# Kernel tuning notes

Measured on AMD Instinct MI355X. Metric: run time of the kernel, lower is better.

The kernel has to match this reference:

```python
import jax, jax.numpy as jnp
import numpy as np

N, F, K, E = 65536, 256, 8, 2097152  # nodes, feat dim, experts, edges (avg degree 32)


def setup_inputs() -> dict:
    key = jax.random.key(0)
    ks = jax.random.split(key, 7)
    x = jax.random.normal(ks[0], (N, F), dtype=jnp.float32)
    h0 = jax.random.normal(ks[1], (N, F), dtype=jnp.float32)
    z = jax.random.uniform(ks[2], (N, K), dtype=jnp.float32)
    rows = jax.random.randint(ks[3], (E,), 0, N, dtype=jnp.int32)
    cols = jax.random.randint(ks[4], (E,), 0, N, dtype=jnp.int32)
    # normalized-ish edge weights (like sym-normalized adjacency values)
    vals = jax.random.uniform(ks[5], (E,), dtype=jnp.float32) / 32.0
    stdv = 1.0 / np.sqrt(F)  # reset_parameters: uniform(-stdv, stdv), stdv = 1/sqrt(out)
    weights = jax.random.uniform(ks[6], (K, F, F), minval=-stdv, maxval=stdv, dtype=jnp.float32)
    return {"x": x, "h0": h0, "z": z, "vals": vals, "weights": weights,
            "rows": rows, "cols": cols}


def reference(x, h0, z, vals, weights, rows, cols):
    # hi = spmm(adj, x): irregular gather + segment-sum over edge list
    hi = jax.ops.segment_sum(vals[:, None] * x[cols], rows, num_segments=N)  # [N,F]
    # variant=False: support = hi. Fused K-expert combine:
    # torch: outputs[k] = support @ W[k]; out = sum_k z[:,k,None] * outputs[k]
    out = jnp.einsum('ni,kio,nk->no', hi, weights, z)  # [N,F]
    # residual=True
    return out + x
```

## Files before the change

kernel.cpp:

```cpp
#include <hip/hip_runtime.h>
#include <hip/hip_bf16.h>

using short8 = __attribute__((ext_vector_type(8))) short;
using f32x4  = __attribute__((ext_vector_type(4))) float;
using f32x2  = __attribute__((ext_vector_type(2))) float;
typedef unsigned int u32;

static constexpr int NN = 65536;
static constexpr int F  = 256;
static constexpr int KE = 8;
static constexpr int KD = KE * F;
static constexpr int NB = 256;
static constexpr int EPB = 8192;
static constexpr int BCAP = 12288;

__device__ __forceinline__ short f2bf(float f) {
    union { __hip_bfloat16 h; short s; } u;
    u.h = __float2bfloat16(f);
    return u.s;
}

__global__ __launch_bounds__(256)
void conv_x8(const float* __restrict__ x, u32* __restrict__ xq,
             int* __restrict__ bcursor) {
    if (blockIdx.x == 0 && threadIdx.x < NB)
        bcursor[threadIdx.x] = threadIdx.x * BCAP;
    const size_t i = ((size_t)blockIdx.x * 256 + threadIdx.x) * 8;
    const float4 a = *(const float4*)(x + i);
    const float4 b = *(const float4*)(x + i + 4);
    u32 w0 = __builtin_amdgcn_cvt_pk_fp8_f32(a.x, a.y, 0, false);
    w0     = __builtin_amdgcn_cvt_pk_fp8_f32(a.z, a.w, w0, true);
    u32 w1 = __builtin_amdgcn_cvt_pk_fp8_f32(b.x, b.y, 0, false);
    w1     = __builtin_amdgcn_cvt_pk_fp8_f32(b.z, b.w, w1, true);
    *(uint2*)(xq + i / 4) = make_uint2(w0, w1);
}

__global__ void prep_w(const float* __restrict__ W, short* __restrict__ WbT) {
    __shared__ float tile[64][65];
    const int e   = blockIdx.z;
    const int i0b = blockIdx.x;
    const int wc  = blockIdx.y;
    const int c  = threadIdx.x & 63;
    const int r4 = threadIdx.x >> 6;
    for (int rr = r4; rr < 64; rr += 4)
        tile[rr][c] = W[((size_t)e * F + i0b * 64 + rr) * F + wc * 64 + c];
    __syncthreads();
    const int s = e * 4 + i0b;
    #pragma unroll
    for (int q = 0; q < 2; ++q) {
        const int ci   = threadIdx.x + q * 256;
        const int nk   = ci >> 6;
        const int lane = ci & 63;
        const int ni = nk >> 1, ks = nk & 1;
        const int hi2 = lane >> 4, lr = lane & 15;
        const int o_l = ni * 16 + lr;
        const int i_l = ks * 32 + hi2 * 8;
        short8 pk;
        #pragma unroll
        for (int j = 0; j < 8; ++j) pk[j] = f2bf(tile[i_l + j][o_l]);
        *(short8*)(WbT + ((((size_t)(wc * 32 + s) * 8 + nk) << 6) + lane) * 8) = pk;
    }
}

__global__ __launch_bounds__(256)
void bucket_scatter(const int* __restrict__ rows, const int* __restrict__ cols,
                    const float* __restrict__ vals, int* __restrict__ bcursor,
                    int2* __restrict__ tmp, int E) {
    __shared__ int h[NB], wb[NB];
    const int tid = threadIdx.x;
    h[tid] = 0;
    __syncthreads();
    const int base = blockIdx.x * EPB;
    const int lim  = min(EPB, E - base);
    for (int i = tid; i < lim; i += 256)
        atomicAdd(&h[rows[base + i] >> 8], 1);
    __syncthreads();
    const int c = h[tid];
    wb[tid] = c ? atomicAdd(&bcursor[tid], c) : 0;
    h[tid] = 0;
    __syncthreads();
    for (int i = tid; i < lim; i += 256) {
        const int r  = rows[base + i];
        const int bk = r >> 8;
        const int rank = atomicAdd(&h[bk], 1);
        tmp[wb[bk] + rank] = make_int2(((r & 255) << 16) | cols[base + i],
                                       __float_as_int(vals[base + i]));
    }
}

__global__ __launch_bounds__(256)
void bucket_to_csr(const int* __restrict__ bcursor, int2* __restrict__ tmp,
                   int* __restrict__ offsets, int* __restrict__ rend) {
    __shared__ int2 buf[BCAP];
    __shared__ int h[NB], off[NB];
    const int tid = threadIdx.x;
    const int k   = blockIdx.x;
    const int beg = k * BCAP;
    const int n   = bcursor[k] - beg;
    h[tid] = 0;
    __syncthreads();
    for (int i = tid; i < n; i += 256) {
        const int2 e = tmp[beg + i];
        if (i < BCAP) buf[i] = e;
        atomicAdd(&h[e.x >> 16], 1);
    }
    __syncthreads();
    const int c = h[tid];
    off[tid] = c;
    __syncthreads();
    for (int o = 1; o < NB; o <<= 1) {
        int v = (tid >= o) ? off[tid - o] : 0;
        __syncthreads();
        off[tid] += v;
        __syncthreads();
    }
    const int excl = off[tid] - c;
    offsets[k * NB + tid] = beg + excl;
    rend[k * NB + tid]    = beg + excl + c;
    h[tid] = excl;
    __syncthreads();
    for (int i = tid; i < n; i += 256) {
        const int2 e = (i < BCAP) ? buf[i] : tmp[beg + i];
        const int r = e.x >> 16;
        const int pos = atomicAdd(&h[r], 1);
        tmp[beg + pos] = make_int2(e.x & 0xFFFF, e.y);
    }
}

__global__ __launch_bounds__(256)
void gather_rows(const u32* __restrict__ xq, const int2* __restrict__ scv,
                 const int* __restrict__ offsets, const int* __restrict__ rend,
                 float* __restrict__ hi) {
    const int lane = threadIdx.x & 63;
    int row = (blockIdx.x << 2) + (threadIdx.x >> 6);
    row = __builtin_amdgcn_readfirstlane(row);
    const int beg = offsets[row];
    const int end = rend[row];
    float4 acc = {0.f, 0.f, 0.f, 0.f};
    int j = beg;
    for (; j + 8 <= end; j += 8) {
        int2 cc[8];
        u32  rr[8];
        #pragma unroll
        for (int q = 0; q < 8; ++q) cc[q] = scv[j + q];
        #pragma unroll
        for (int q = 0; q < 8; ++q)
            rr[q] = (xq + (size_t)cc[q].x * (F / 4))[lane];
        #pragma unroll
        for (int q = 0; q < 8; ++q) {
            const float v = __int_as_float(cc[q].y);
            const f32x2 lo = __builtin_amdgcn_cvt_pk_f32_fp8(rr[q], false);
            const f32x2 hi2 = __builtin_amdgcn_cvt_pk_f32_fp8(rr[q], true);
            acc.x += v * lo[0];  acc.y += v * lo[1];
            acc.z += v * hi2[0]; acc.w += v * hi2[1];
        }
    }
    for (; j < end; ++j) {
        const int2 c0 = scv[j];
        const u32 r0 = (xq + (size_t)c0.x * (F / 4))[lane];
        const float v0 = __int_as_float(c0.y);
        const f32x2 lo = __builtin_amdgcn_cvt_pk_f32_fp8(r0, false);
        const f32x2 hi2 = __builtin_amdgcn_cvt_pk_f32_fp8(r0, true);
        acc.x += v0 * lo[0];  acc.y += v0 * lo[1];
        acc.z += v0 * hi2[0]; acc.w += v0 * hi2[1];
    }
    ((float4*)(hi + (size_t)row * F))[lane] = acc;
}

#define BM 128
__global__ __launch_bounds__(1024, 4)
void moe_gemm(const float* __restrict__ hi, const float* __restrict__ z,
              const short* __restrict__ WbT, const float* __restrict__ x,
              float* __restrict__ out) {
    __shared__ short A_lds[4][BM * 64];
    __shared__ float z_t[KE][BM];
    const int tid  = threadIdx.x;
    const int lane = tid & 63;
    const int w    = tid >> 6;
    const int wr   = w >> 2;
    const int wc   = w & 3;
    const int row0 = blockIdx.x * BM;

    z_t[tid & 7][tid >> 3] = z[(size_t)row0 * KE + tid];
    {
        const int m0 = tid >> 5;
        const int c8 = tid & 31;
        for (int p = 0; p < BM / 32; ++p) {
            const int m = p * 32 + m0;
            const float4* src = (const float4*)(hi + (size_t)(row0 + m) * F + c8 * 8);
            const float4 a = src[0], b = src[1];
            short8 pk;
            pk[0]=f2bf(a.x); pk[1]=f2bf(a.y); pk[2]=f2bf(a.z); pk[3]=f2bf(a.w);
            pk[4]=f2bf(b.x); pk[5]=f2bf(b.y); pk[6]=f2bf(b.z); pk[7]=f2bf(b.w);
            const int byte = m * 128 + (((c8 & 7) * 16) ^ ((m & 7) << 4));
            *(short8*)((char*)&A_lds[c8 >> 3][0] + byte) = pk;
        }
    }
    __syncthreads();

    f32x4 acc_t[2][4];
    #pragma unroll
    for (int mi = 0; mi < 2; ++mi)
        #pragma unroll
        for (int ni = 0; ni < 4; ++ni)
            acc_t[mi][ni] = (f32x4){0.f, 0.f, 0.f, 0.f};

    const int lr    = lane & 15;
    const int kq16  = (lane >> 4) * 16;
    const int rbase = (lane >> 4) * 4;

    const short* Bw = WbT + ((size_t)wc * 256 << 9) + lane * 8;

    #pragma unroll 1
    for (int s = 0; s < 32; ++s) {
        const int e = s >> 2;

        short8 bf[8];
        const short* ps = Bw + ((size_t)s * 8 << 9);
        #pragma unroll
        for (int nk = 0; nk < 8; ++nk)
            bf[nk] = *(const short8*)(ps + ((size_t)nk << 9));

        #pragma unroll
        for (int mi = 0; mi < 2; ++mi) {
            const int m = wr * 32 + mi * 16 + lr;
            short8 af[2];
            #pragma unroll
            for (int ks = 0; ks < 2; ++ks) {
                const int slot = ks * 64 + kq16;
                af[ks] = *(const short8*)((const char*)&A_lds[s & 3][0]
                            + m * 128 + (slot ^ ((m & 7) << 4)));
            }
            f32x4 pe[4];
            #pragma unroll
            for (int ni = 0; ni < 4; ++ni) pe[ni] = (f32x4){0.f, 0.f, 0.f, 0.f};
            #pragma unroll
            for (int ks = 0; ks < 2; ++ks)
                #pragma unroll
                for (int ni = 0; ni < 4; ++ni)
                    pe[ni] = __builtin_amdgcn_mfma_f32_16x16x32_bf16(
                        af[ks], bf[ni * 2 + ks], pe[ni], 0, 0, 0);
            const f32x4 zv = *(const f32x4*)&z_t[e][wr * 32 + mi * 16 + rbase];
            #pragma unroll
            for (int ni = 0; ni < 4; ++ni)
                #pragma unroll
                for (int r = 0; r < 4; ++r)
                    acc_t[mi][ni][r] += zv[r] * pe[ni][r];
        }
    }

    #pragma unroll
    for (int mi = 0; mi < 2; ++mi) {
        #pragma unroll
        for (int r = 0; r < 4; ++r) {
            const int m = wr * 32 + mi * 16 + rbase + r;
            const size_t rowoff = (size_t)(row0 + m) * F;
            #pragma unroll
            for (int ni = 0; ni < 4; ++ni) {
                const int o = wc * 64 + ni * 16 + lr;
                out[rowoff + o] = acc_t[mi][ni][r] + x[rowoff + o];
            }
        }
    }
}

extern "C" void kernel_launch(void* const* d_in, const int* in_sizes, int n_in,
                              void* d_out, int out_size, void* d_ws, size_t ws_size,
                              hipStream_t stream) {
    const float* x    = (const float*)d_in[0];
    const float* z    = (const float*)d_in[2];
    const float* vals = (const float*)d_in[3];
    const float* W    = (const float*)d_in[4];
    const int* rows   = (const int*)d_in[5];
    const int* cols   = (const int*)d_in[6];
    float* out        = (float*)d_out;
    const int E = in_sizes[3];

    char* ws = (char*)d_ws;
    u32*   xq      = (u32*)  (ws);
    short* WbT     = (short*)(ws + ((size_t)16 << 20));
    int*   offsets = (int*)  (ws + ((size_t)17 << 20));
    int*   rend    = (int*)  (ws + ((size_t)17 << 20) + 256*1024);
    int*   bcursor = (int*)  (ws + ((size_t)17 << 20) + 512*1024);
    int2*  tmp     = (int2*) (ws + ((size_t)18 << 20));
    float* hi      = out;

    const int nblk = (E + EPB - 1) / EPB;
    conv_x8<<<(NN * F) / (256 * 8), 256, 0, stream>>>(x, xq, bcursor);
    prep_w<<<dim3(4, 4, 8), 256, 0, stream>>>(W, WbT);
    bucket_scatter<<<nblk, 256, 0, stream>>>(rows, cols, vals, bcursor, tmp, E);
    bucket_to_csr<<<NB, 256, 0, stream>>>(bcursor, tmp, offsets, rend);
    gather_rows<<<NN / 4, 256, 0, stream>>>(xq, tmp, offsets, rend, hi);
    moe_gemm<<<NN / BM, 1024, 0, stream>>>(hi, z, WbT, x, out);
}
```

Measured before the change: 242.1 us.

## Switch MoE GEMM to FP8 MFMA with FP8 hidden features and weights

Stores the aggregated hidden features from gather_rows as FP8 in a separate workspace buffer instead of FP32 in the output buffer, and packs the expert weights as FP8. The GEMM uses the 16x16x32 fp8 MFMA and a byte-wide swizzled LDS layout. This cuts the hidden write and read traffic by a factor of four and halves weight and LDS bandwidth. The cost is lower accuracy, since FP8 (e4m3) quantizes both the activations and the weights, which may exceed tolerance.

```diff
diff --git a/kernel.cpp b/kernel.cpp
--- a/kernel.cpp
+++ b/kernel.cpp
@@ -4,20 +4,19 @@
 using short8 = __attribute__((ext_vector_type(8))) short;
 using f32x4  = __attribute__((ext_vector_type(4))) float;
 using f32x2  = __attribute__((ext_vector_type(2))) float;
+using long2v = __attribute__((ext_vector_type(2))) long;
 typedef unsigned int u32;
 
 static constexpr int NN = 65536;
 static constexpr int F  = 256;
 static constexpr int KE = 8;
-static constexpr int KD = KE * F;
 static constexpr int NB = 256;
 static constexpr int EPB = 8192;
 static constexpr int BCAP = 12288;
 
-__device__ __forceinline__ short f2bf(float f) {
-    union { __hip_bfloat16 h; short s; } u;
-    u.h = __float2bfloat16(f);
-    return u.s;
+__device__ __forceinline__ u32 pk4_fp8(float a, float b, float c, float d) {
+    u32 p = __builtin_amdgcn_cvt_pk_fp8_f32(a, b, 0, false);
+    return __builtin_amdgcn_cvt_pk_fp8_f32(c, d, p, true);
 }
 
 __global__ __launch_bounds__(256)
@@ -28,14 +27,11 @@
     const size_t i = ((size_t)blockIdx.x * 256 + threadIdx.x) * 8;
     const float4 a = *(const float4*)(x + i);
     const float4 b = *(const float4*)(x + i + 4);
-    u32 w0 = __builtin_amdgcn_cvt_pk_fp8_f32(a.x, a.y, 0, false);
-    w0     = __builtin_amdgcn_cvt_pk_fp8_f32(a.z, a.w, w0, true);
-    u32 w1 = __builtin_amdgcn_cvt_pk_fp8_f32(b.x, b.y, 0, false);
-    w1     = __builtin_amdgcn_cvt_pk_fp8_f32(b.z, b.w, w1, true);
-    *(uint2*)(xq + i / 4) = make_uint2(w0, w1);
-}
-
-__global__ void prep_w(const float* __restrict__ W, short* __restrict__ WbT) {
+    *(uint2*)(xq + i / 4) = make_uint2(pk4_fp8(a.x, a.y, a.z, a.w),
+                                       pk4_fp8(b.x, b.y, b.z, b.w));
+}
+
+__global__ void prep_w(const float* __restrict__ W, u32* __restrict__ WbT8) {
     __shared__ float tile[64][65];
     const int e   = blockIdx.z;
     const int i0b = blockIdx.x;
@@ -45,21 +41,22 @@
     for (int rr = r4; rr < 64; rr += 4)
         tile[rr][c] = W[((size_t)e * F + i0b * 64 + rr) * F + wc * 64 + c];
     __syncthreads();
-    const int s = e * 4 + i0b;
+    const int s    = e * 4 + i0b;
+    const int ni   = threadIdx.x >> 6;
+    const int lane = threadIdx.x & 63;
+    const int hi2 = lane >> 4, lr = lane & 15;
+    const int o_l = ni * 16 + lr;
+    uint4 outv;
+    u32* ov = (u32*)&outv;
     #pragma unroll
-    for (int q = 0; q < 2; ++q) {
-        const int ci   = threadIdx.x + q * 256;
-        const int nk   = ci >> 6;
-        const int lane = ci & 63;
-        const int ni = nk >> 1, ks = nk & 1;
-        const int hi2 = lane >> 4, lr = lane & 15;
-        const int o_l = ni * 16 + lr;
+    for (int ks = 0; ks < 2; ++ks) {
         const int i_l = ks * 32 + hi2 * 8;
-        short8 pk;
-        #pragma unroll
-        for (int j = 0; j < 8; ++j) pk[j] = f2bf(tile[i_l + j][o_l]);
-        *(short8*)(WbT + ((((size_t)(wc * 32 + s) * 8 + nk) << 6) + lane) * 8) = pk;
-    }
+        ov[ks * 2 + 0] = pk4_fp8(tile[i_l + 0][o_l], tile[i_l + 1][o_l],
+                                 tile[i_l + 2][o_l], tile[i_l + 3][o_l]);
+        ov[ks * 2 + 1] = pk4_fp8(tile[i_l + 4][o_l], tile[i_l + 5][o_l],
+                                 tile[i_l + 6][o_l], tile[i_l + 7][o_l]);
+    }
+    *(uint4*)((char*)WbT8 + (((size_t)(wc * 32 + s) * 4 + ni) << 10) + lane * 16) = outv;
 }
 
 __global__ __launch_bounds__(256)
@@ -130,7 +127,7 @@
 __global__ __launch_bounds__(256)
 void gather_rows(const u32* __restrict__ xq, const int2* __restrict__ scv,
                  const int* __restrict__ offsets, const int* __restrict__ rend,
-                 float* __restrict__ hi) {
+                 u32* __restrict__ hiq) {
     const int lane = threadIdx.x & 63;
     int row = (blockIdx.x << 2) + (threadIdx.x >> 6);
     row = __builtin_amdgcn_readfirstlane(row);
@@ -164,15 +161,15 @@
         acc.x += v0 * lo[0];  acc.y += v0 * lo[1];
         acc.z += v0 * hi2[0]; acc.w += v0 * hi2[1];
     }
-    ((float4*)(hi + (size_t)row * F))[lane] = acc;
+    hiq[(size_t)row * 64 + lane] = pk4_fp8(acc.x, acc.y, acc.z, acc.w);
 }
 
 #define BM 128
 __global__ __launch_bounds__(1024, 4)
-void moe_gemm(const float* __restrict__ hi, const float* __restrict__ z,
-              const short* __restrict__ WbT, const float* __restrict__ x,
+void moe_gemm(const u32* __restrict__ hiq, const float* __restrict__ z,
+              const u32* __restrict__ WbT8, const float* __restrict__ x,
               float* __restrict__ out) {
-    __shared__ short A_lds[4][BM * 64];
+    __shared__ char A_lds[4][BM * 64];
     __shared__ float z_t[KE][BM];
     const int tid  = threadIdx.x;
     const int lane = tid & 63;
@@ -183,17 +180,14 @@
 
     z_t[tid & 7][tid >> 3] = z[(size_t)row0 * KE + tid];
     {
-        const int m0 = tid >> 5;
-        const int c8 = tid & 31;
-        for (int p = 0; p < BM / 32; ++p) {
-            const int m = p * 32 + m0;
-            const float4* src = (const float4*)(hi + (size_t)(row0 + m) * F + c8 * 8);
-            const float4 a = src[0], b = src[1];
-            short8 pk;
-            pk[0]=f2bf(a.x); pk[1]=f2bf(a.y); pk[2]=f2bf(a.z); pk[3]=f2bf(a.w);
-            pk[4]=f2bf(b.x); pk[5]=f2bf(b.y); pk[6]=f2bf(b.z); pk[7]=f2bf(b.w);
-            const int byte = m * 128 + (((c8 & 7) * 16) ^ ((m & 7) << 4));
-            *(short8*)((char*)&A_lds[c8 >> 3][0] + byte) = pk;
+        for (int p = 0; p < 4; ++p) {
+            const int u    = p * 1024 + tid;
+            const int m    = u >> 5;
+            const int ku8  = u & 31;
+            const int sl   = ku8 >> 3;
+            const int slot = ku8 & 7;
+            const uint2 v = *(const uint2*)(hiq + (size_t)(row0 + m) * 64 + ku8 * 2);
+            *(uint2*)(&A_lds[sl][0] + m * 64 + ((slot ^ (m & 7)) << 3)) = v;
         }
     }
     __syncthreads();
@@ -206,30 +200,30 @@
             acc_t[mi][ni] = (f32x4){0.f, 0.f, 0.f, 0.f};
 
     const int lr    = lane & 15;
-    const int kq16  = (lane >> 4) * 16;
-    const int rbase = (lane >> 4) * 4;
-
-    const short* Bw = WbT + ((size_t)wc * 256 << 9) + lane * 8;
+    const int hi2   = lane >> 4;
+    const int rbase = hi2 * 4;
+
+    const char* Bw = (const char*)WbT8 + (((size_t)wc * 32 * 4) << 10) + lane * 16;
 
     #pragma unroll 1
     for (int s = 0; s < 32; ++s) {
         const int e = s >> 2;
 
-        short8 bf[8];
-        const short* ps = Bw + ((size_t)s * 8 << 9);
-        #pragma unroll
-        for (int nk = 0; nk < 8; ++nk)
-            bf[nk] = *(const short8*)(ps + ((size_t)nk << 9));
+        long2v bf[4];
+        const char* ps = Bw + ((size_t)s * 4 << 10);
+        #pragma unroll
+        for (int ni = 0; ni < 4; ++ni)
+            bf[ni] = *(const long2v*)(ps + ((size_t)ni << 10));
 
         #pragma unroll
         for (int mi = 0; mi < 2; ++mi) {
             const int m = wr * 32 + mi * 16 + lr;
-            short8 af[2];
+            long af[2];
             #pragma unroll
             for (int ks = 0; ks < 2; ++ks) {
-                const int slot = ks * 64 + kq16;
-                af[ks] = *(const short8*)((const char*)&A_lds[s & 3][0]
-                            + m * 128 + (slot ^ ((m & 7) << 4)));
+                const int slot = ks * 4 + hi2;
+                af[ks] = *(const long*)(&A_lds[s & 3][0]
+                            + m * 64 + ((slot ^ (m & 7)) << 3));
             }
             f32x4 pe[4];
             #pragma unroll
@@ -238,8 +232,8 @@
             for (int ks = 0; ks < 2; ++ks)
                 #pragma unroll
                 for (int ni = 0; ni < 4; ++ni)
-                    pe[ni] = __builtin_amdgcn_mfma_f32_16x16x32_bf16(
-                        af[ks], bf[ni * 2 + ks], pe[ni], 0, 0, 0);
+                    pe[ni] = __builtin_amdgcn_mfma_f32_16x16x32_fp8_fp8(
+                        af[ks], ks ? bf[ni].y : bf[ni].x, pe[ni], 0, 0, 0);
             const f32x4 zv = *(const f32x4*)&z_t[e][wr * 32 + mi * 16 + rbase];
             #pragma unroll
             for (int ni = 0; ni < 4; ++ni)
@@ -278,18 +272,18 @@
 
     char* ws = (char*)d_ws;
     u32*   xq      = (u32*)  (ws);
-    short* WbT     = (short*)(ws + ((size_t)16 << 20));
+    u32*   WbT8    = (u32*)  (ws + ((size_t)16 << 20));
     int*   offsets = (int*)  (ws + ((size_t)17 << 20));
     int*   rend    = (int*)  (ws + ((size_t)17 << 20) + 256*1024);
     int*   bcursor = (int*)  (ws + ((size_t)17 << 20) + 512*1024);
     int2*  tmp     = (int2*) (ws + ((size_t)18 << 20));
-    float* hi      = out;
+    u32*   hiq     = (u32*)  (ws + ((size_t)42 << 20));
 
     const int nblk = (E + EPB - 1) / EPB;
     conv_x8<<<(NN * F) / (256 * 8), 256, 0, stream>>>(x, xq, bcursor);
-    prep_w<<<dim3(4, 4, 8), 256, 0, stream>>>(W, WbT);
+    prep_w<<<dim3(4, 4, 8), 256, 0, stream>>>(W, WbT8);
     bucket_scatter<<<nblk, 256, 0, stream>>>(rows, cols, vals, bcursor, tmp, E);
     bucket_to_csr<<<NB, 256, 0, stream>>>(bcursor, tmp, offsets, rend);
-    gather_rows<<<NN / 4, 256, 0, stream>>>(xq, tmp, offsets, rend, hi);
-    moe_gemm<<<NN / BM, 1024, 0, stream>>>(hi, z, WbT, x, out);
-}
+    gather_rows<<<NN / 4, 256, 0, stream>>>(xq, tmp, offsets, rend, hiq);
+    moe_gemm<<<NN / BM, 1024, 0, stream>>>(hiq, z, WbT8, x, out);
+}
```

Measured after the change: 203.9 us. 1.19x faster.
